# Performance work log

Hardware: AMD Instinct MI355X
Metric: run time of the kernel (lower is better)

The kernel has to match this reference:

```python
import jax, jax.numpy as jnp
import numpy as np

VOCAB = 32000
EMBED = 512
DEP_SIZE = 64
QKV = 512
B, S = 16, 1024
NEG = -1e10


def setup_inputs() -> dict:
    key = jax.random.key(0)
    ks = jax.random.split(key, 16)
    inputs = jax.random.randint(ks[0], (B, S), 0, VOCAB)
    dependency = jax.random.randint(ks[1], (B, S, S), 0, DEP_SIZE)
    embed_table = jax.random.normal(ks[2], (VOCAB, EMBED), dtype=jnp.float32) * 0.02
    dep_table = jax.random.normal(ks[3], (DEP_SIZE, 1), dtype=jnp.float32) * 0.02
    dep_table = dep_table.at[0].set(0.0)  # padding_idx=0
    sc = 1.0 / np.sqrt(EMBED)
    Wq = jax.random.normal(ks[4], (EMBED, QKV), dtype=jnp.float32) * sc
    bq = jnp.zeros((QKV,), jnp.float32)
    Wk = jax.random.normal(ks[5], (EMBED, QKV), dtype=jnp.float32) * sc
    bk = jnp.zeros((QKV,), jnp.float32)
    Wv = jax.random.normal(ks[6], (EMBED, QKV), dtype=jnp.float32) * sc
    bv = jnp.zeros((QKV,), jnp.float32)
    scv = 1.0 / np.sqrt(QKV)
    W1 = jax.random.normal(ks[7], (QKV, QKV), dtype=jnp.float32) * scv
    b1 = jnp.zeros((QKV,), jnp.float32)
    W2 = jax.random.normal(ks[8], (QKV, QKV), dtype=jnp.float32) * scv
    b2 = jnp.zeros((QKV,), jnp.float32)
    return dict(inputs=inputs, dependency=dependency, embed_table=embed_table,
                dep_table=dep_table, Wq=Wq, bq=bq, Wk=Wk, bk=bk, Wv=Wv, bv=bv,
                W1=W1, b1=b1, W2=W2, b2=b2)


def reference(inputs, dependency, embed_table, dep_table, Wq, bq, Wk, bk, Wv, bv, W1, b1, W2, b2):
    x = jnp.take(embed_table, inputs, axis=0)                  # [B,S,E]
    dep_emb = jnp.take(dep_table, dependency, axis=0)[..., 0]  # [B,S,S]
    q = x @ Wq + bq                                            # [B,S,D]
    k = x @ Wk + bk
    v = x @ Wv + bv
    attn = jnp.einsum('bqd,bkd->bqk', q, k) * dep_emb          # [B,S,S]
    attn = jnp.where(dependency == 0, NEG, attn)
    weights = jax.nn.softmax(attn, axis=-1)
    wm = jnp.einsum('bqk,bkd->bqd', weights, v)                # fused weighted sum
    wm = jnp.tanh(wm @ W1 + b1) @ W2 + b2
    return wm, weights
```

## Files before the change

kernel.cpp:

```cpp
#include <hip/hip_runtime.h>

typedef __attribute__((ext_vector_type(8))) short short8;
typedef __attribute__((ext_vector_type(4))) float floatx4;

__device__ __forceinline__ unsigned short f2b(float f) {
  unsigned int u = __float_as_uint(f);
  unsigned int r = (u + 0x7FFFu + ((u >> 16) & 1u)) >> 16;
  return (unsigned short)r;
}
__device__ __forceinline__ uint4 ld8f(const float* p) {
  float4 a = *(const float4*)p;
  float4 b = *(const float4*)(p + 4);
  uint4 r;
  r.x = (unsigned int)f2b(a.x) | ((unsigned int)f2b(a.y) << 16);
  r.y = (unsigned int)f2b(a.z) | ((unsigned int)f2b(a.w) << 16);
  r.z = (unsigned int)f2b(b.x) | ((unsigned int)f2b(b.y) << 16);
  r.w = (unsigned int)f2b(b.z) | ((unsigned int)f2b(b.w) << 16);
  return r;
}

#define GLL(g, l) __builtin_amdgcn_global_load_lds( \
    (const __attribute__((address_space(1))) unsigned int*)(g), \
    (__attribute__((address_space(3))) unsigned int*)(l), 16, 0, 0)

__device__ __forceinline__ void kloop(const unsigned short* __restrict__ A,
                                      const unsigned short* __restrict__ B,
                                      int K, unsigned short* ldsA, unsigned short* ldsB,
                                      floatx4 (&acc)[4][4])
{
  const int tid = threadIdx.x;
  const int w = tid >> 6, lane = tid & 63;
  const int quad = lane >> 4, l16 = lane & 15;
  const int wy = w >> 1, wx = w & 1;
  const int rs = 32 * w + (lane >> 2);
  const int ks = (lane & 3) * 8;
  const int lo0 = (w * 2) * 512 + lane * 8;
  const int lo1 = lo0 + 512;
  const unsigned short* a0 = A + (size_t)rs * K + ks;
  const unsigned short* a1 = a0 + (size_t)16 * K;
  const unsigned short* b0 = B + (size_t)rs * K + ks;
  const unsigned short* b1 = b0 + (size_t)16 * K;

  for (int k0 = 0; k0 < K; k0 += 32) {
    __syncthreads();
    GLL(a0 + k0, &ldsA[lo0]);
    GLL(a1 + k0, &ldsA[lo1]);
    GLL(b0 + k0, &ldsB[lo0]);
    GLL(b1 + k0, &ldsB[lo1]);
    __syncthreads();
    short8 af[4], bf[4];
#pragma unroll
    for (int i = 0; i < 4; i++)
      af[i] = *(const short8*)&ldsA[(wy * 64 + i * 16 + l16) * 32 + quad * 8];
#pragma unroll
    for (int j = 0; j < 4; j++)
      bf[j] = *(const short8*)&ldsB[(wx * 64 + j * 16 + l16) * 32 + quad * 8];
#pragma unroll
    for (int i = 0; i < 4; i++)
#pragma unroll
      for (int j = 0; j < 4; j++)
        acc[i][j] = __builtin_amdgcn_mfma_f32_16x16x32_bf16(af[i], bf[j], acc[i][j], 0, 0, 0);
  }
}

__global__ __launch_bounds__(256, 2) void gemm_qkv(
    const unsigned short* __restrict__ x,
    const unsigned short* __restrict__ WT,
    const float* __restrict__ bq, const float* __restrict__ bk, const float* __restrict__ bv,
    unsigned short* __restrict__ q, unsigned short* __restrict__ kx, unsigned short* __restrict__ v)
{
  __shared__ unsigned short ldsA[4096], ldsB[4096];
  const int m0 = blockIdx.y * 128, n0 = blockIdx.x * 128;
  floatx4 acc[4][4];
#pragma unroll
  for (int i = 0; i < 4; i++)
#pragma unroll
    for (int j = 0; j < 4; j++) acc[i][j] = (floatx4){0.f, 0.f, 0.f, 0.f};

  kloop(x + (size_t)m0 * 512, WT + (size_t)n0 * 512, 512, ldsA, ldsB, acc);

  const int seg = n0 >> 9, nloc = n0 & 511;
  unsigned short* C = seg == 0 ? q : (seg == 1 ? kx : v);
  const float* bias = seg == 0 ? bq : (seg == 1 ? bk : bv);
  const int lane = threadIdx.x & 63, w = threadIdx.x >> 6;
  const int quad = lane >> 4, l16 = lane & 15, wy = w >> 1, wx = w & 1;
  float bvv[4];
#pragma unroll
  for (int j = 0; j < 4; j++) bvv[j] = bias[nloc + wx * 64 + j * 16 + l16];
#pragma unroll
  for (int i = 0; i < 4; i++)
#pragma unroll
    for (int r = 0; r < 4; r++) {
      int m = m0 + wy * 64 + i * 16 + quad * 4 + r;
      unsigned short* crow = C + (size_t)m * 512 + nloc + wx * 64 + l16;
#pragma unroll
      for (int j = 0; j < 4; j++) crow[j * 16] = f2b(acc[i][j][r] + bvv[j]);
    }
}

template<int CF32, int ACT>
__global__ __launch_bounds__(256, 2) void gemm2(
    const unsigned short* __restrict__ A, const unsigned short* __restrict__ Bt,
    const float* __restrict__ bias, void* __restrict__ Cv,
    int N, int K, long aB, long bB, long cB)
{
  __shared__ unsigned short ldsA[4096], ldsB[4096];
  const int b = blockIdx.z;
  const int m0 = blockIdx.y * 128, n0 = blockIdx.x * 128;
  floatx4 acc[4][4];
#pragma unroll
  for (int i = 0; i < 4; i++)
#pragma unroll
    for (int j = 0; j < 4; j++) acc[i][j] = (floatx4){0.f, 0.f, 0.f, 0.f};

  kloop(A + (size_t)b * aB + (size_t)m0 * K, Bt + (size_t)b * bB + (size_t)n0 * K,
        K, ldsA, ldsB, acc);

  const int lane = threadIdx.x & 63, w = threadIdx.x >> 6;
  const int quad = lane >> 4, l16 = lane & 15, wy = w >> 1, wx = w & 1;
  float bvv[4];
#pragma unroll
  for (int j = 0; j < 4; j++)
    bvv[j] = bias ? bias[n0 + wx * 64 + j * 16 + l16] : 0.f;
  float*          Cf = (float*)Cv          + (size_t)b * cB;
  unsigned short* Ch = (unsigned short*)Cv + (size_t)b * cB;
#pragma unroll
  for (int i = 0; i < 4; i++)
#pragma unroll
    for (int r = 0; r < 4; r++) {
      int m = m0 + wy * 64 + i * 16 + quad * 4 + r;
      size_t base = (size_t)m * N + n0 + wx * 64 + l16;
#pragma unroll
      for (int j = 0; j < 4; j++) {
        float vv = acc[i][j][r] + bvv[j];
        if (ACT == 1) vv = tanhf(vv);
        if (CF32) Cf[base + j * 16] = vv;
        else      Ch[base + j * 16] = f2b(vv);
      }
    }
}

#define CST 132
__global__ __launch_bounds__(256, 2) void score_kernel(
    const unsigned short* __restrict__ Q, const unsigned short* __restrict__ Km,
    const int* __restrict__ dep, const float* __restrict__ dept,
    float* __restrict__ E)
{
  __shared__ union {
    struct { unsigned short a[4096]; unsigned short b[4096]; } s;
    float c[32 * CST];
  } sm;
  __shared__ float dtab[64];
  const int tid = threadIdx.x;
  if (tid < 64) dtab[tid] = dept[tid];

  const int b = blockIdx.z;
  const int m0 = blockIdx.y * 128, n0 = blockIdx.x * 128;
  floatx4 acc[4][4];
#pragma unroll
  for (int i = 0; i < 4; i++)
#pragma unroll
    for (int j = 0; j < 4; j++) acc[i][j] = (floatx4){0.f, 0.f, 0.f, 0.f};

  kloop(Q + (size_t)b * (1024 * 512) + (size_t)m0 * 512,
        Km + (size_t)b * (1024 * 512) + (size_t)n0 * 512,
        512, sm.s.a, sm.s.b, acc);

  const int lane = tid & 63, w = tid >> 6;
  const int quad = lane >> 4, l16 = lane & 15, wy = w >> 1, wx = w & 1;
  const int* depb = dep + (size_t)b * 1024 * 1024;
  float* Eb = E + (size_t)b * 1024 * 1024;
  const int cr = tid >> 3, cb = (tid & 7) * 16;

#pragma unroll
  for (int i = 0; i < 4; i++) {
    __syncthreads();
#pragma unroll
    for (int j = 0; j < 4; j++)
#pragma unroll
      for (int r = 0; r < 4; r++)
        sm.c[(wy * 16 + quad * 4 + r) * CST + wx * 64 + j * 16 + l16] = acc[i][j][r];
    __syncthreads();
    const int m = m0 + (cr >> 4) * 64 + i * 16 + (cr & 15);
    const int* dr = depb + (size_t)m * 1024 + n0 + cb;
    float* er = Eb + (size_t)m * 1024 + n0 + cb;
    const float* crow = &sm.c[cr * CST + cb];
#pragma unroll
    for (int c = 0; c < 4; c++) {
      int4 d = *(const int4*)(dr + c * 4);
      float4 s = *(const float4*)(crow + c * 4);
      float4 e;
      e.x = d.x ? __expf(fminf(fmaxf(s.x * dtab[d.x & 63], -60.f), 60.f)) : 0.f;
      e.y = d.y ? __expf(fminf(fmaxf(s.y * dtab[d.y & 63], -60.f), 60.f)) : 0.f;
      e.z = d.z ? __expf(fminf(fmaxf(s.z * dtab[d.z & 63], -60.f), 60.f)) : 0.f;
      e.w = d.w ? __expf(fminf(fmaxf(s.w * dtab[d.w & 63], -60.f), 60.f)) : 0.f;
      *(float4*)(er + c * 4) = e;
    }
  }
}

__global__ void build_x(const float* __restrict__ embed, const int* __restrict__ inputs,
                        unsigned short* __restrict__ x)
{
  const int row = blockIdx.x * 4 + (threadIdx.x >> 6);
  const int lane = threadIdx.x & 63;
  const float* src = embed + (size_t)inputs[row] * 512 + lane * 8;
  *(uint4*)&x[(size_t)row * 512 + lane * 8] = ld8f(src);
}

__global__ void trans_w(const float* s0, const float* s1, const float* s2,
                        const float* s3, const float* s4, unsigned short* dst)
{
  __shared__ unsigned short tile[32][33];
  const int z = blockIdx.z;
  const float* src = z == 0 ? s0 : z == 1 ? s1 : z == 2 ? s2 : z == 3 ? s3 : s4;
  unsigned short* ob = dst + (size_t)z * 262144;
  int c0 = blockIdx.x * 32, r0 = blockIdx.y * 32;
  int tx = threadIdx.x & 31, ty = threadIdx.x >> 5;
  for (int i = ty; i < 32; i += 8)
    tile[i][tx] = f2b(src[(size_t)(r0 + i) * 512 + (c0 + tx)]);
  __syncthreads();
  for (int i = ty; i < 32; i += 8)
    ob[(size_t)(c0 + i) * 512 + (r0 + tx)] = tile[tx][i];
}

__global__ void trans_v(const unsigned short* __restrict__ in, unsigned short* __restrict__ out)
{
  __shared__ unsigned short tile[32][33];
  const unsigned short* ib = in + (size_t)blockIdx.z * (1024 * 512);
  unsigned short* ob = out + (size_t)blockIdx.z * (512 * 1024);
  int c0 = blockIdx.x * 32, r0 = blockIdx.y * 32;
  int tx = threadIdx.x & 31, ty = threadIdx.x >> 5;
  for (int i = ty; i < 32; i += 8)
    tile[i][tx] = ib[(size_t)(r0 + i) * 512 + (c0 + tx)];
  __syncthreads();
  for (int i = ty; i < 32; i += 8)
    ob[(size_t)(c0 + i) * 1024 + (r0 + tx)] = tile[tx][i];
}

__global__ void normalize_rows(float* __restrict__ wf, unsigned short* __restrict__ wb)
{
  size_t row = blockIdx.x;
  float4* p = (float4*)(wf + row * 1024);
  float4 u = p[threadIdx.x];
  float s = (u.x + u.y) + (u.z + u.w);
#pragma unroll
  for (int d = 1; d < 64; d <<= 1) s += __shfl_xor(s, d);
  __shared__ float acc4[4];
  if ((threadIdx.x & 63) == 0) acc4[threadIdx.x >> 6] = s;
  __syncthreads();
  float tot = (acc4[0] + acc4[1]) + (acc4[2] + acc4[3]);
  float inv = tot > 0.f ? 1.f / tot : 0.f;
  u.x *= inv; u.y *= inv; u.z *= inv; u.w *= inv;
  p[threadIdx.x] = u;
  uint2 pk;
  pk.x = (unsigned int)f2b(u.x) | ((unsigned int)f2b(u.y) << 16);
  pk.y = (unsigned int)f2b(u.z) | ((unsigned int)f2b(u.w) << 16);
  *(uint2*)&wb[row * 1024 + threadIdx.x * 4] = pk;
}

extern "C" void kernel_launch(void* const* d_in, const int* in_sizes, int n_in,
                              void* d_out, int out_size, void* d_ws, size_t ws_size,
                              hipStream_t stream)
{
  const int*   inputs     = (const int*)d_in[0];
  const int*   dependency = (const int*)d_in[1];
  const float* embed      = (const float*)d_in[2];
  const float* dept       = (const float*)d_in[3];
  const float* Wq = (const float*)d_in[4];   const float* bq = (const float*)d_in[5];
  const float* Wk = (const float*)d_in[6];   const float* bk = (const float*)d_in[7];
  const float* Wv = (const float*)d_in[8];   const float* bvv = (const float*)d_in[9];
  const float* W1 = (const float*)d_in[10];  const float* b1 = (const float*)d_in[11];
  const float* W2 = (const float*)d_in[12];  const float* b2 = (const float*)d_in[13];

  float* out  = (float*)d_out;
  float* wout = out + (size_t)8388608;

  unsigned short* ws   = (unsigned short*)d_ws;
  unsigned short* q    = ws;
  unsigned short* kx   = ws + 8388608;
  unsigned short* WTc  = ws + 16777216;
  unsigned short* W1T  = ws + 17563648;
  unsigned short* W2T  = ws + 17825792;
  unsigned short* wbf  = ws;
  unsigned short* h    = ws;

  unsigned short* x    = (unsigned short*)wout;
  unsigned short* v    = (unsigned short*)out;
  unsigned short* vT   = (unsigned short*)out + 8388608;
  unsigned short* wmp  = (unsigned short*)out;

  dim3 blk(256);

  trans_w<<<dim3(16, 16, 5), blk, 0, stream>>>(Wq, Wk, Wv, W1, W2, WTc);
  build_x<<<dim3(4096), blk, 0, stream>>>(embed, inputs, x);

  gemm_qkv<<<dim3(12, 128, 1), blk, 0, stream>>>(x, WTc, bq, bk, bvv, q, kx, v);

  score_kernel<<<dim3(8, 8, 16), blk, 0, stream>>>(q, kx, dependency, dept, wout);

  trans_v<<<dim3(16, 32, 16), blk, 0, stream>>>(v, vT);

  normalize_rows<<<dim3(16384), blk, 0, stream>>>(wout, wbf);

  gemm2<0, 0><<<dim3(4, 8, 16), blk, 0, stream>>>(wbf, vT, nullptr, wmp,
                                                  512, 1024, 1024L * 1024, 512L * 1024, 1024L * 512);
  gemm2<0, 1><<<dim3(4, 128, 1), blk, 0, stream>>>(wmp, W1T, b1, h, 512, 512, 0, 0, 0);
  gemm2<1, 0><<<dim3(4, 128, 1), blk, 0, stream>>>(h, W2T, b2, out, 512, 512, 0, 0, 0);
}
```

Before: 406.1 us.

## Shrink GEMM tiles to 64x128, raise occupancy, add XCD-aware block swizzle

All bf16 GEMM kernels (QKV projection, score, PV, MLP) move from 128x128 to 64x128 output tiles. Each wave now holds a 2x4 accumulator array instead of 4x4, and the launch bounds rise to 4 blocks per CU, so grids double in size. This is meant to fix poor wave occupancy and grid under-fill, for example 1024 blocks on 256 CUs. A block-index swizzle spreads consecutive logical blocks across the 8 XCDs to improve L2 locality. The cost is lower arithmetic intensity per tile and more global/LDS traffic for the B operand.

```diff
diff --git a/kernel.cpp b/kernel.cpp
--- a/kernel.cpp
+++ b/kernel.cpp
@@ -23,57 +23,67 @@
     (const __attribute__((address_space(1))) unsigned int*)(g), \
     (__attribute__((address_space(3))) unsigned int*)(l), 16, 0, 0)
 
+__device__ __forceinline__ void xcd_swz(int& bx, int& by, int& bz) {
+  const int nx = gridDim.x, ny = gridDim.y;
+  const int nwg = nx * ny * gridDim.z;
+  const int lbid = blockIdx.x + nx * (blockIdx.y + ny * blockIdx.z);
+  const int s = (lbid & 7) * (nwg >> 3) + (lbid >> 3);
+  bx = s % nx; by = (s / nx) % ny; bz = s / (nx * ny);
+}
+
 __device__ __forceinline__ void kloop(const unsigned short* __restrict__ A,
                                       const unsigned short* __restrict__ B,
                                       int K, unsigned short* ldsA, unsigned short* ldsB,
-                                      floatx4 (&acc)[4][4])
+                                      floatx4 (&acc)[2][4])
 {
   const int tid = threadIdx.x;
   const int w = tid >> 6, lane = tid & 63;
   const int quad = lane >> 4, l16 = lane & 15;
   const int wy = w >> 1, wx = w & 1;
-  const int rs = 32 * w + (lane >> 2);
+  const int rsa = 16 * w + (lane >> 2);
+  const int rsb = 32 * w + (lane >> 2);
   const int ks = (lane & 3) * 8;
-  const int lo0 = (w * 2) * 512 + lane * 8;
-  const int lo1 = lo0 + 512;
-  const unsigned short* a0 = A + (size_t)rs * K + ks;
-  const unsigned short* a1 = a0 + (size_t)16 * K;
-  const unsigned short* b0 = B + (size_t)rs * K + ks;
+  const int loa  = w * 512 + lane * 8;
+  const int lob0 = w * 1024 + lane * 8;
+  const int lob1 = lob0 + 512;
+  const unsigned short* a0 = A + (size_t)rsa * K + ks;
+  const unsigned short* b0 = B + (size_t)rsb * K + ks;
   const unsigned short* b1 = b0 + (size_t)16 * K;
 
   for (int k0 = 0; k0 < K; k0 += 32) {
     __syncthreads();
-    GLL(a0 + k0, &ldsA[lo0]);
-    GLL(a1 + k0, &ldsA[lo1]);
-    GLL(b0 + k0, &ldsB[lo0]);
-    GLL(b1 + k0, &ldsB[lo1]);
+    GLL(a0 + k0, &ldsA[loa]);
+    GLL(b0 + k0, &ldsB[lob0]);
+    GLL(b1 + k0, &ldsB[lob1]);
     __syncthreads();
-    short8 af[4], bf[4];
-#pragma unroll
-    for (int i = 0; i < 4; i++)
-      af[i] = *(const short8*)&ldsA[(wy * 64 + i * 16 + l16) * 32 + quad * 8];
+    short8 af[2], bf[4];
+#pragma unroll
+    for (int i = 0; i < 2; i++)
+      af[i] = *(const short8*)&ldsA[(wy * 32 + i * 16 + l16) * 32 + quad * 8];
 #pragma unroll
     for (int j = 0; j < 4; j++)
       bf[j] = *(const short8*)&ldsB[(wx * 64 + j * 16 + l16) * 32 + quad * 8];
 #pragma unroll
-    for (int i = 0; i < 4; i++)
+    for (int i = 0; i < 2; i++)
 #pragma unroll
       for (int j = 0; j < 4; j++)
         acc[i][j] = __builtin_amdgcn_mfma_f32_16x16x32_bf16(af[i], bf[j], acc[i][j], 0, 0, 0);
   }
 }
 
-__global__ __launch_bounds__(256, 2) void gemm_qkv(
+__global__ __launch_bounds__(256, 4) void gemm_qkv(
     const unsigned short* __restrict__ x,
     const unsigned short* __restrict__ WT,
     const float* __restrict__ bq, const float* __restrict__ bk, const float* __restrict__ bv,
     unsigned short* __restrict__ q, unsigned short* __restrict__ kx, unsigned short* __restrict__ v)
 {
-  __shared__ unsigned short ldsA[4096], ldsB[4096];
-  const int m0 = blockIdx.y * 128, n0 = blockIdx.x * 128;
-  floatx4 acc[4][4];
-#pragma unroll
-  for (int i = 0; i < 4; i++)
+  __shared__ unsigned short ldsA[2048], ldsB[4096];
+  int bx, by, bz;
+  xcd_swz(bx, by, bz);
+  const int m0 = by * 64, n0 = bx * 128;
+  floatx4 acc[2][4];
+#pragma unroll
+  for (int i = 0; i < 2; i++)
 #pragma unroll
     for (int j = 0; j < 4; j++) acc[i][j] = (floatx4){0.f, 0.f, 0.f, 0.f};
 
@@ -88,10 +98,10 @@
 #pragma unroll
   for (int j = 0; j < 4; j++) bvv[j] = bias[nloc + wx * 64 + j * 16 + l16];
 #pragma unroll
-  for (int i = 0; i < 4; i++)
+  for (int i = 0; i < 2; i++)
 #pragma unroll
     for (int r = 0; r < 4; r++) {
-      int m = m0 + wy * 64 + i * 16 + quad * 4 + r;
+      int m = m0 + wy * 32 + i * 16 + quad * 4 + r;
       unsigned short* crow = C + (size_t)m * 512 + nloc + wx * 64 + l16;
 #pragma unroll
       for (int j = 0; j < 4; j++) crow[j * 16] = f2b(acc[i][j][r] + bvv[j]);
@@ -99,17 +109,19 @@
 }
 
 template<int CF32, int ACT>
-__global__ __launch_bounds__(256, 2) void gemm2(
+__global__ __launch_bounds__(256, 4) void gemm2(
     const unsigned short* __restrict__ A, const unsigned short* __restrict__ Bt,
     const float* __restrict__ bias, void* __restrict__ Cv,
     int N, int K, long aB, long bB, long cB)
 {
-  __shared__ unsigned short ldsA[4096], ldsB[4096];
-  const int b = blockIdx.z;
-  const int m0 = blockIdx.y * 128, n0 = blockIdx.x * 128;
-  floatx4 acc[4][4];
-#pragma unroll
-  for (int i = 0; i < 4; i++)
+  __shared__ unsigned short ldsA[2048], ldsB[4096];
+  int bx, by, bz;
+  xcd_swz(bx, by, bz);
+  const int b = bz;
+  const int m0 = by * 64, n0 = bx * 128;
+  floatx4 acc[2][4];
+#pragma unroll
+  for (int i = 0; i < 2; i++)
 #pragma unroll
     for (int j = 0; j < 4; j++) acc[i][j] = (floatx4){0.f, 0.f, 0.f, 0.f};
 
@@ -125,10 +137,10 @@
   float*          Cf = (float*)Cv          + (size_t)b * cB;
   unsigned short* Ch = (unsigned short*)Cv + (size_t)b * cB;
 #pragma unroll
-  for (int i = 0; i < 4; i++)
+  for (int i = 0; i < 2; i++)
 #pragma unroll
     for (int r = 0; r < 4; r++) {
-      int m = m0 + wy * 64 + i * 16 + quad * 4 + r;
+      int m = m0 + wy * 32 + i * 16 + quad * 4 + r;
       size_t base = (size_t)m * N + n0 + wx * 64 + l16;
 #pragma unroll
       for (int j = 0; j < 4; j++) {
@@ -141,24 +153,26 @@
 }
 
 #define CST 132
-__global__ __launch_bounds__(256, 2) void score_kernel(
+__global__ __launch_bounds__(256, 4) void score_kernel(
     const unsigned short* __restrict__ Q, const unsigned short* __restrict__ Km,
     const int* __restrict__ dep, const float* __restrict__ dept,
     float* __restrict__ E)
 {
   __shared__ union {
-    struct { unsigned short a[4096]; unsigned short b[4096]; } s;
+    struct { unsigned short a[2048]; unsigned short b[4096]; } s;
     float c[32 * CST];
   } sm;
   __shared__ float dtab[64];
   const int tid = threadIdx.x;
   if (tid < 64) dtab[tid] = dept[tid];
 
-  const int b = blockIdx.z;
-  const int m0 = blockIdx.y * 128, n0 = blockIdx.x * 128;
-  floatx4 acc[4][4];
-#pragma unroll
-  for (int i = 0; i < 4; i++)
+  int bx, by, bz;
+  xcd_swz(bx, by, bz);
+  const int b = bz;
+  const int m0 = by * 64, n0 = bx * 128;
+  floatx4 acc[2][4];
+#pragma unroll
+  for (int i = 0; i < 2; i++)
 #pragma unroll
     for (int j = 0; j < 4; j++) acc[i][j] = (floatx4){0.f, 0.f, 0.f, 0.f};
 
@@ -173,7 +187,7 @@
   const int cr = tid >> 3, cb = (tid & 7) * 16;
 
 #pragma unroll
-  for (int i = 0; i < 4; i++) {
+  for (int i = 0; i < 2; i++) {
     __syncthreads();
 #pragma unroll
     for (int j = 0; j < 4; j++)
@@ -181,7 +195,7 @@
       for (int r = 0; r < 4; r++)
         sm.c[(wy * 16 + quad * 4 + r) * CST + wx * 64 + j * 16 + l16] = acc[i][j][r];
     __syncthreads();
-    const int m = m0 + (cr >> 4) * 64 + i * 16 + (cr & 15);
+    const int m = m0 + (cr >> 4) * 32 + i * 16 + (cr & 15);
     const int* dr = depb + (size_t)m * 1024 + n0 + cb;
     float* er = Eb + (size_t)m * 1024 + n0 + cb;
     const float* crow = &sm.c[cr * CST + cb];
@@ -295,16 +309,16 @@
   trans_w<<<dim3(16, 16, 5), blk, 0, stream>>>(Wq, Wk, Wv, W1, W2, WTc);
   build_x<<<dim3(4096), blk, 0, stream>>>(embed, inputs, x);
 
-  gemm_qkv<<<dim3(12, 128, 1), blk, 0, stream>>>(x, WTc, bq, bk, bvv, q, kx, v);
-
-  score_kernel<<<dim3(8, 8, 16), blk, 0, stream>>>(q, kx, dependency, dept, wout);
+  gemm_qkv<<<dim3(12, 256, 1), blk, 0, stream>>>(x, WTc, bq, bk, bvv, q, kx, v);
+
+  score_kernel<<<dim3(8, 16, 16), blk, 0, stream>>>(q, kx, dependency, dept, wout);
 
   trans_v<<<dim3(16, 32, 16), blk, 0, stream>>>(v, vT);
 
   normalize_rows<<<dim3(16384), blk, 0, stream>>>(wout, wbf);
 
-  gemm2<0, 0><<<dim3(4, 8, 16), blk, 0, stream>>>(wbf, vT, nullptr, wmp,
-                                                  512, 1024, 1024L * 1024, 512L * 1024, 1024L * 512);
-  gemm2<0, 1><<<dim3(4, 128, 1), blk, 0, stream>>>(wmp, W1T, b1, h, 512, 512, 0, 0, 0);
-  gemm2<1, 0><<<dim3(4, 128, 1), blk, 0, stream>>>(h, W2T, b2, out, 512, 512, 0, 0, 0);
-}
+  gemm2<0, 0><<<dim3(4, 16, 16), blk, 0, stream>>>(wbf, vT, nullptr, wmp,
+                                                   512, 1024, 1024L * 1024, 512L * 1024, 1024L * 512);
+  gemm2<0, 1><<<dim3(4, 256, 1), blk, 0, stream>>>(wmp, W1T, b1, h, 512, 512, 0, 0, 0);
+  gemm2<1, 0><<<dim3(4, 256, 1), blk, 0, stream>>>(h, W2T, b2, out, 512, 512, 0, 0, 0);
+}
```

After: 400.2 us. No clear change (-1.4%).
